# Kernel tuning notes

Measured on AMD Instinct MI355X. Metric: run time of the kernel, lower is better.

Reference implementation:

```python
import jax, jax.numpy as jnp
import numpy as np

B, S, D = 8, 1024, 1152
H = 16
HD = D // H
HID = int(D * 4.0)
LN_EPS = 1e-5


def layer_norm(x, w, b):
    m = jnp.mean(x, axis=-1, keepdims=True)
    v = jnp.mean(jnp.square(x - m), axis=-1, keepdims=True)
    return (x - m) * jax.lax.rsqrt(v + LN_EPS) * w + b


def modulate(x, shift, scale):
    # shift/scale: [B, D] broadcast over seq
    return x * (1.0 + scale[:, None, :]) + shift[:, None, :]


def setup_inputs() -> dict:
    key = jax.random.key(0)
    ks = jax.random.split(key, 16)
    s = 0.02
    return {
        "x": jax.random.normal(ks[0], (B, S, D), jnp.float32),
        "c": jax.random.normal(ks[1], (B, D), jnp.float32),
        "ln1_w": jnp.ones((D,), jnp.float32),
        "ln1_b": jnp.zeros((D,), jnp.float32),
        "wq": jax.random.normal(ks[2], (D, D), jnp.float32) * s,
        "wk": jax.random.normal(ks[3], (D, D), jnp.float32) * s,
        "wv": jax.random.normal(ks[4], (D, D), jnp.float32) * s,
        "wo": jax.random.normal(ks[5], (D, D), jnp.float32) * s,
        "wo_b": jnp.zeros((D,), jnp.float32),
        "ln2_w": jnp.ones((D,), jnp.float32),
        "ln2_b": jnp.zeros((D,), jnp.float32),
        "fc1_w": jax.random.normal(ks[6], (D, HID), jnp.float32) * s,
        "fc1_b": jnp.zeros((HID,), jnp.float32),
        "fc2_w": jax.random.normal(ks[7], (HID, D), jnp.float32) * s,
        "fc2_b": jnp.zeros((D,), jnp.float32),
        "ada_w": jax.random.normal(ks[8], (D, 6 * D), jnp.float32) * s,
        "ada_b": jnp.zeros((6 * D,), jnp.float32),
    }


def attention(x, wq, wk, wv, wo, wo_b):
    b, s, d = x.shape
    q = (x @ wq).reshape(b, s, H, HD).transpose(0, 2, 1, 3)  # [B,H,S,hd]
    k = (x @ wk).reshape(b, s, H, HD).transpose(0, 2, 1, 3)
    v = (x @ wv).reshape(b, s, H, HD).transpose(0, 2, 1, 3)
    scale = 1.0 / np.sqrt(HD).astype(np.float32)
    att = jnp.einsum("bhqd,bhkd->bhqk", q, k) * scale
    att = jax.nn.softmax(att, axis=-1)
    out = jnp.einsum("bhqk,bhkd->bhqd", att, v)
    out = out.transpose(0, 2, 1, 3).reshape(b, s, d)
    return out @ wo + wo_b


def reference(x, c, ln1_w, ln1_b, wq, wk, wv, wo, wo_b, ln2_w, ln2_b,
              fc1_w, fc1_b, fc2_w, fc2_b, ada_w, ada_b):
    mod = jax.nn.silu(c) @ ada_w + ada_b  # [B, 6D]
    sh_msa, sc_msa, g_msa, sh_mlp, sc_mlp, g_mlp = jnp.split(mod, 6, axis=1)
    h = modulate(layer_norm(x, ln1_w, ln1_b), sh_msa, sc_msa)
    x = x + g_msa[:, None, :] * attention(h, wq, wk, wv, wo, wo_b)
    h = modulate(layer_norm(x, ln2_w, ln2_b), sh_mlp, sc_mlp)
    h = jax.nn.gelu(h @ fc1_w + fc1_b, approximate=False) @ fc2_w + fc2_b
    x = x + g_mlp[:, None, :] * h
    return x
```

## Files before the change

kernel.cpp:

```cpp
#include <hip/hip_runtime.h>
#include <hip/hip_bf16.h>


typedef unsigned short u16;
typedef unsigned int u32;
typedef __attribute__((ext_vector_type(8))) short bf16x8;
typedef __attribute__((ext_vector_type(4))) float f32x4;

#define MFMA16(a, b, c) __builtin_amdgcn_mfma_f32_16x16x32_bf16((a), (b), (c), 0, 0, 0)

__device__ __forceinline__ u16 f2bf(float f) {
  __hip_bfloat16 h = __float2bfloat16(f);
  return __builtin_bit_cast(u16, h);
}

__device__ __forceinline__ void gload16(const u16* g, u16* l) {
  __builtin_amdgcn_global_load_lds(
      (const __attribute__((address_space(1))) unsigned int*)(const void*)g,
      (__attribute__((address_space(3))) unsigned int*)(void*)l, 16, 0, 0);
}

__global__ void k_silu(const float* __restrict__ c, float* __restrict__ o, int n) {
  int i = blockIdx.x * 256 + threadIdx.x;
  if (i < n) { float v = c[i]; o[i] = v / (1.f + __expf(-v)); }
}

__global__ __launch_bounds__(256) void k_modproj1(const float* __restrict__ sc,
                                                  const float* __restrict__ aw,
                                                  float* __restrict__ partial) {
  __shared__ float lc[8][144];
  int kc = blockIdx.y;
  for (int i = threadIdx.x; i < 1152; i += 256) {
    int b = i / 144, k = i % 144;
    lc[b][k] = sc[b * 1152 + kc * 144 + k];
  }
  __syncthreads();
  int j = blockIdx.x * 256 + threadIdx.x;
  float acc[8] = {0, 0, 0, 0, 0, 0, 0, 0};
  for (int k = 0; k < 144; ++k) {
    float w = aw[(size_t)(kc * 144 + k) * 6912 + j];
    #pragma unroll
    for (int b = 0; b < 8; ++b) acc[b] += lc[b][k] * w;
  }
  #pragma unroll
  for (int b = 0; b < 8; ++b) partial[((size_t)kc * 8 + b) * 6912 + j] = acc[b];
}

__global__ __launch_bounds__(256) void k_modproj2(const float* __restrict__ partial,
                                                  const float* __restrict__ ab,
                                                  float* __restrict__ mo) {
  int j = blockIdx.x * 256 + threadIdx.x;
  float bias = ab[j];
  #pragma unroll
  for (int b = 0; b < 8; ++b) {
    float s = 0.f;
    #pragma unroll
    for (int kc = 0; kc < 8; ++kc) s += partial[((size_t)kc * 8 + b) * 6912 + j];
    mo[(size_t)b * 6912 + j] = s + bias;
  }
}

__global__ __launch_bounds__(256) void k_tcvt(const float* __restrict__ in, u16* __restrict__ out,
                                              int K, int N) {
  __shared__ float t[32][33];
  int tx = threadIdx.x & 31, ty = threadIdx.x >> 5;
  size_t bx = (size_t)blockIdx.x * 32, by = (size_t)blockIdx.y * 32;
  #pragma unroll
  for (int i = 0; i < 4; ++i) t[ty + 8 * i][tx] = in[(by + ty + 8 * i) * N + bx + tx];
  __syncthreads();
  #pragma unroll
  for (int i = 0; i < 4; ++i) out[(bx + ty + 8 * i) * K + by + tx] = f2bf(t[tx][ty + 8 * i]);
}

__global__ __launch_bounds__(256) void k_lnmod(const float* __restrict__ xin,
                                               const float* __restrict__ w,
                                               const float* __restrict__ bs,
                                               const float* __restrict__ mo,
                                               int sh_off, int sc_off, u16* __restrict__ o) {
  int row = blockIdx.x;
  int b = row >> 10;
  int tid = threadIdx.x;
  const float4* x4 = (const float4*)(xin + (size_t)row * 1152);
  float4 v0 = x4[tid];
  float4 v1 = make_float4(0.f, 0.f, 0.f, 0.f);
  if (tid < 32) v1 = x4[256 + tid];
  float s = v0.x + v0.y + v0.z + v0.w + v1.x + v1.y + v1.z + v1.w;
  float sq = v0.x * v0.x + v0.y * v0.y + v0.z * v0.z + v0.w * v0.w +
             v1.x * v1.x + v1.y * v1.y + v1.z * v1.z + v1.w * v1.w;
  #pragma unroll
  for (int d = 32; d > 0; d >>= 1) { s += __shfl_down(s, d); sq += __shfl_down(sq, d); }
  __shared__ float ps[4], pq[4];
  int wid = tid >> 6, lane = tid & 63;
  if (lane == 0) { ps[wid] = s; pq[wid] = sq; }
  __syncthreads();
  float S = ps[0] + ps[1] + ps[2] + ps[3];
  float SQ = pq[0] + pq[1] + pq[2] + pq[3];
  float mean = S * (1.f / 1152.f);
  float var = SQ * (1.f / 1152.f) - mean * mean;
  float rs = rsqrtf(var + 1e-5f);
  const float* shp = mo + (size_t)b * 6912 + sh_off;
  const float* scp = mo + (size_t)b * 6912 + sc_off;
  u16* orow = o + (size_t)row * 1152;
  {
    int col = 4 * tid;
    ushort4 u; float y;
    y = (v0.x - mean) * rs * w[col + 0] + bs[col + 0]; u.x = f2bf(y * (1.f + scp[col + 0]) + shp[col + 0]);
    y = (v0.y - mean) * rs * w[col + 1] + bs[col + 1]; u.y = f2bf(y * (1.f + scp[col + 1]) + shp[col + 1]);
    y = (v0.z - mean) * rs * w[col + 2] + bs[col + 2]; u.z = f2bf(y * (1.f + scp[col + 2]) + shp[col + 2]);
    y = (v0.w - mean) * rs * w[col + 3] + bs[col + 3]; u.w = f2bf(y * (1.f + scp[col + 3]) + shp[col + 3]);
    *(ushort4*)&orow[col] = u;
  }
  if (tid < 32) {
    int col = 1024 + 4 * tid;
    ushort4 u; float y;
    y = (v1.x - mean) * rs * w[col + 0] + bs[col + 0]; u.x = f2bf(y * (1.f + scp[col + 0]) + shp[col + 0]);
    y = (v1.y - mean) * rs * w[col + 1] + bs[col + 1]; u.y = f2bf(y * (1.f + scp[col + 1]) + shp[col + 1]);
    y = (v1.z - mean) * rs * w[col + 2] + bs[col + 2]; u.z = f2bf(y * (1.f + scp[col + 2]) + shp[col + 2]);
    y = (v1.w - mean) * rs * w[col + 3] + bs[col + 3]; u.w = f2bf(y * (1.f + scp[col + 3]) + shp[col + 3]);
    *(ushort4*)&orow[col] = u;
  }
}

template <int EPI>
__global__ __launch_bounds__(256) void k_gemm(const u16* __restrict__ A, const u16* __restrict__ Bt,
                                              int Kst, int klen, u16* __restrict__ Cb,
                                              float* __restrict__ Cf,
                                              const float* __restrict__ bias,
                                              const float* __restrict__ res,
                                              const float* __restrict__ mo, int goff,
                                              u16* __restrict__ vt) {
  const int tid = threadIdx.x;
  const int w = tid >> 6, lane = tid & 63;
  const int wr = w >> 1, wc = w & 1;
  const int lr = lane & 15, kg = lane >> 4;

  const int nwg = gridDim.x * gridDim.y;
  const int id = blockIdx.y * gridDim.x + blockIdx.x;
  const int swz = (id & 7) * (nwg >> 3) + (id >> 3);
  const int tM = (swz / gridDim.x) * 128, tN = (swz % gridDim.x) * 128;
  const int N = gridDim.x * 128;
  const int koff = blockIdx.z * klen;

  __shared__ u16 lA[2][128 * 32];
  __shared__ u16 lB[2][128 * 32];
  f32x4 acc[4][4];
  #pragma unroll
  for (int m = 0; m < 4; ++m)
    #pragma unroll
    for (int n = 0; n < 4; ++n) acc[m][n] = f32x4{0.f, 0.f, 0.f, 0.f};

  const int lrow = lane >> 2, lseg = lane & 3;
  const u16* gA = A + (size_t)(tM + w * 32 + lrow) * Kst + lseg * 8 + koff;
  const u16* gB = Bt + (size_t)(tN + w * 32 + lrow) * Kst + lseg * 8 + koff;
  const size_t rstep = (size_t)16 * Kst;
  const int wo0 = (w * 32) * 32, wo1 = (w * 32 + 16) * 32;
  const int aoff = (wr * 64 + lr) * 32 + kg * 8;
  const int boff = (wc * 64 + lr) * 32 + kg * 8;

#define STAGE(buf, ks)                        \
  do {                                        \
    gload16(gA + (ks), lA[buf] + wo0);        \
    gload16(gA + rstep + (ks), lA[buf] + wo1);\
    gload16(gB + (ks), lB[buf] + wo0);        \
    gload16(gB + rstep + (ks), lB[buf] + wo1);\
  } while (0)

#define COMPUTE(buf)                                                                  \
  do {                                                                                \
    bf16x8 af[4], bfr[4];                                                             \
    _Pragma("unroll")                                                                 \
    for (int m = 0; m < 4; ++m) af[m] = *(const bf16x8*)&lA[buf][aoff + m * 16 * 32]; \
    _Pragma("unroll")                                                                 \
    for (int n = 0; n < 4; ++n) bfr[n] = *(const bf16x8*)&lB[buf][boff + n * 16 * 32];\
    _Pragma("unroll")                                                                 \
    for (int m = 0; m < 4; ++m)                                                       \
      _Pragma("unroll")                                                               \
      for (int n = 0; n < 4; ++n) acc[m][n] = MFMA16(af[m], bfr[n], acc[m][n]);       \
  } while (0)

  const int nt = klen >> 5;
  STAGE(0, 0);
  __syncthreads();
  int t = 1;
  for (; t + 1 < nt; t += 2) {
    STAGE(1, t * 32);
    COMPUTE(0);
    __syncthreads();
    STAGE(0, t * 32 + 32);
    COMPUTE(1);
    __syncthreads();
  }
  STAGE(1, t * 32);
  COMPUTE(0);
  __syncthreads();
  COMPUTE(1);
#undef STAGE
#undef COMPUTE

  if (EPI == 3) {
    #pragma unroll
    for (int m = 0; m < 4; ++m)
      #pragma unroll
      for (int n = 0; n < 4; ++n) {
        int gcol = tN + wc * 64 + n * 16 + lr;
        int s0 = tM + wr * 64 + m * 16 + kg * 4;
        if (tN < 2304) {
          #pragma unroll
          for (int r = 0; r < 4; ++r) Cb[(size_t)(s0 + r) * N + gcol] = f2bf(acc[m][n][r]);
        } else {
          int qq = gcol - 2304;
          int hh = qq / 72;
          int d = qq - hh * 72;
          int bb = s0 >> 10, sl = s0 & 1023;
          ushort4 u;
          u.x = f2bf(acc[m][n][0]); u.y = f2bf(acc[m][n][1]);
          u.z = f2bf(acc[m][n][2]); u.w = f2bf(acc[m][n][3]);
          *(ushort4*)&vt[(((size_t)bb * 16 + hh) * 72 + d) * 1024 + sl] = u;
        }
      }
  } else if (EPI == 4) {
    float* Po = Cf + (size_t)blockIdx.z * ((size_t)gridDim.y * 128) * N;
    #pragma unroll
    for (int m = 0; m < 4; ++m)
      #pragma unroll
      for (int n = 0; n < 4; ++n)
        #pragma unroll
        for (int r = 0; r < 4; ++r) {
          int grow = tM + wr * 64 + m * 16 + kg * 4 + r;
          int gcol = tN + wc * 64 + n * 16 + lr;
          Po[(size_t)grow * N + gcol] = acc[m][n][r];
        }
  } else {
    #pragma unroll
    for (int m = 0; m < 4; ++m)
      #pragma unroll
      for (int n = 0; n < 4; ++n)
        #pragma unroll
        for (int r = 0; r < 4; ++r) {
          int grow = tM + wr * 64 + m * 16 + kg * 4 + r;
          int gcol = tN + wc * 64 + n * 16 + lr;
          size_t idx = (size_t)grow * N + gcol;
          float v = acc[m][n][r];
          if (EPI == 1) {
            float g = mo[(size_t)(grow >> 10) * 6912 + goff + gcol];
            Cf[idx] = res[idx] + g * (v + bias[gcol]);
          } else {
            float z = v + bias[gcol];
            float z2 = z * z;
            float u = z * __fmaf_rn(z2, -0.0713548162f, -1.5957691216f);
            float e = __expf(u);
            float gel = z * __builtin_amdgcn_rcpf(1.f + e);
            Cb[idx] = f2bf(gel);
          }
        }
  }
}

__global__ __launch_bounds__(256) void k_fc2red(const float* __restrict__ p,
                                                const float* __restrict__ x1,
                                                const float* __restrict__ bias,
                                                const float* __restrict__ mo,
                                                float* __restrict__ out) {
  size_t i = ((size_t)blockIdx.x * 256 + threadIdx.x) * 4;
  int row = (int)(i / 1152);
  int col = (int)(i - (size_t)row * 1152);
  int b = row >> 10;
  float4 a0 = *(const float4*)(p + i);
  float4 a1 = *(const float4*)(p + 9437184ull + i);
  float4 r = *(const float4*)(x1 + i);
  const float* gp = mo + (size_t)b * 6912 + 5760 + col;
  const float* bp = bias + col;
  float4 o;
  o.x = r.x + gp[0] * (a0.x + a1.x + bp[0]);
  o.y = r.y + gp[1] * (a0.y + a1.y + bp[1]);
  o.z = r.z + gp[2] * (a0.z + a1.z + bp[2]);
  o.w = r.w + gp[3] * (a0.w + a1.w + bp[3]);
  *(float4*)(out + i) = o;
}

__global__ __launch_bounds__(256) void k_attn(const u16* __restrict__ QKV, const u16* __restrict__ Vt,
                                              u16* __restrict__ O) {
  const int tid = threadIdx.x;
  const int w = tid >> 6, lane = tid & 63;
  const int lr = lane & 15, kg = lane >> 4;
  int bx = blockIdx.x;
  bx = (bx & 7) * 256 + (bx >> 3);
  const int qt = bx & 15, h = (bx >> 4) & 15, b = bx >> 8;

  __shared__ u16 lQ[64][104];
  __shared__ u16 lK[64][104];
  __shared__ u16 lVt[80][72];
  __shared__ u16 lPt[4][16][72];

  const size_t qkbase = (size_t)b * 1024 * 3456 + (size_t)h * 72;
  const u16* Qg = QKV + qkbase;
  const u16* Kg = QKV + qkbase + 1152;
  const u16* Vg = Vt + ((size_t)(b * 16 + h) * 72) * 1024;

  const uint4 z4 = make_uint4(0, 0, 0, 0);
  for (int L = tid; L < 192; L += 256) {
    int r = L / 3, s = L - (L / 3) * 3;
    *(uint4*)&lQ[r][72 + s * 8] = z4;
    *(uint4*)&lK[r][72 + s * 8] = z4;
  }
  for (int L = tid; L < 72; L += 256) {
    int r = L / 9, s = L - (L / 9) * 9;
    *(uint4*)&lVt[72 + r][s * 8] = z4;
  }
  {
    int L = tid; int r = L / 9, s = L - r * 9;
    *(uint4*)&lQ[r][s * 8] = *(const uint4*)(Qg + (size_t)(qt * 64 + r) * 3456 + s * 8);
    L = tid + 256; r = L / 9; s = L - r * 9;
    *(uint4*)&lQ[r][s * 8] = *(const uint4*)(Qg + (size_t)(qt * 64 + r) * 3456 + s * 8);
    if (tid < 64) {
      L = tid + 512; r = L / 9; s = L - r * 9;
      *(uint4*)&lQ[r][s * 8] = *(const uint4*)(Qg + (size_t)(qt * 64 + r) * 3456 + s * 8);
    }
  }
  __syncthreads();

  bf16x8 bq[3];
  #pragma unroll
  for (int ks = 0; ks < 3; ++ks) bq[ks] = *(const bf16x8*)&lQ[w * 16 + lr][ks * 32 + kg * 8];

  const float scale = 0.11785113019775793f;
  float mrun = -1e30f, lrun = 0.f;
  f32x4 oacc[5];
  #pragma unroll
  for (int nd = 0; nd < 5; ++nd) oacc[nd] = f32x4{0.f, 0.f, 0.f, 0.f};

  for (int kt = 0; kt < 16; ++kt) {
    __syncthreads();
    {
      int L = tid; int r = L / 9, s = L - (L / 9) * 9;
      *(uint4*)&lK[r][s * 8] = *(const uint4*)(Kg + (size_t)(kt * 64 + r) * 3456 + s * 8);
      int d = tid >> 3, sg = tid & 7;
      *(uint4*)&lVt[d][sg * 8] = *(const uint4*)(Vg + (size_t)d * 1024 + kt * 64 + sg * 8);
      L = tid + 256; r = L / 9; s = L - r * 9;
      *(uint4*)&lK[r][s * 8] = *(const uint4*)(Kg + (size_t)(kt * 64 + r) * 3456 + s * 8);
      d = (tid + 256) >> 3; sg = tid & 7;
      *(uint4*)&lVt[d][sg * 8] = *(const uint4*)(Vg + (size_t)d * 1024 + kt * 64 + sg * 8);
      if (tid < 64) {
        L = tid + 512; r = L / 9; s = L - r * 9;
        *(uint4*)&lK[r][s * 8] = *(const uint4*)(Kg + (size_t)(kt * 64 + r) * 3456 + s * 8);
        d = (tid + 512) >> 3;
        *(uint4*)&lVt[d][sg * 8] = *(const uint4*)(Vg + (size_t)d * 1024 + kt * 64 + sg * 8);
      }
    }
    __syncthreads();

    f32x4 sfr[4];
    __builtin_amdgcn_s_setprio(1);
    #pragma unroll
    for (int kb = 0; kb < 4; ++kb) {
      f32x4 sv = f32x4{0.f, 0.f, 0.f, 0.f};
      #pragma unroll
      for (int ks = 0; ks < 3; ++ks) {
        bf16x8 ak = *(const bf16x8*)&lK[kb * 16 + lr][ks * 32 + kg * 8];
        sv = MFMA16(ak, bq[ks], sv);
      }
      sfr[kb] = sv;
    }
    __builtin_amdgcn_s_setprio(0);

    float mx = sfr[0][0];
    #pragma unroll
    for (int kb = 0; kb < 4; ++kb)
      #pragma unroll
      for (int r = 0; r < 4; ++r) mx = fmaxf(mx, sfr[kb][r]);
    mx = fmaxf(mx, __shfl_xor(mx, 16));
    mx = fmaxf(mx, __shfl_xor(mx, 32));
    mx *= scale;
    float mn = fmaxf(mrun, mx);
    float al = __expf(mrun - mn);
    mrun = mn;
    float sum = 0.f;
    #pragma unroll
    for (int kb = 0; kb < 4; ++kb) {
      #pragma unroll
      for (int rp = 0; rp < 2; ++rp) {
        float p0 = __expf(__fmaf_rn(sfr[kb][2 * rp], scale, -mn));
        float p1 = __expf(__fmaf_rn(sfr[kb][2 * rp + 1], scale, -mn));
        sum += p0 + p1;
        u32 pk = (u32)f2bf(p0) | ((u32)f2bf(p1) << 16);
        *(u32*)&lPt[w][lr][kb * 16 + kg * 4 + rp * 2] = pk;
      }
    }
    sum += __shfl_xor(sum, 16);
    sum += __shfl_xor(sum, 32);
    lrun = lrun * al + sum;
    #pragma unroll
    for (int nd = 0; nd < 5; ++nd)
      #pragma unroll
      for (int r = 0; r < 4; ++r) oacc[nd][r] *= al;

    __builtin_amdgcn_s_setprio(1);
    #pragma unroll
    for (int s = 0; s < 2; ++s) {
      bf16x8 bp = *(const bf16x8*)&lPt[w][lr][s * 32 + kg * 8];
      #pragma unroll
      for (int nd = 0; nd < 5; ++nd) {
        bf16x8 av = *(const bf16x8*)&lVt[nd * 16 + lr][s * 32 + kg * 8];
        oacc[nd] = MFMA16(av, bp, oacc[nd]);
      }
    }
    __builtin_amdgcn_s_setprio(0);
  }

  float inv = 1.f / lrun;
  size_t orow = ((size_t)b * 1024 + qt * 64 + w * 16 + lr) * 1152 + h * 72;
  #pragma unroll
  for (int nd = 0; nd < 5; ++nd) {
    int d0 = nd * 16 + kg * 4;
    if (d0 < 72) {
      ushort4 u;
      u.x = f2bf(oacc[nd][0] * inv);
      u.y = f2bf(oacc[nd][1] * inv);
      u.z = f2bf(oacc[nd][2] * inv);
      u.w = f2bf(oacc[nd][3] * inv);
      *(ushort4*)&O[orow + d0] = u;
    }
  }
}

extern "C" void kernel_launch(void* const* d_in, const int* in_sizes, int n_in,
                              void* d_out, int out_size, void* d_ws, size_t ws_size,
                              hipStream_t stream) {
  const float* x     = (const float*)d_in[0];
  const float* c     = (const float*)d_in[1];
  const float* ln1_w = (const float*)d_in[2];
  const float* ln1_b = (const float*)d_in[3];
  const float* wq    = (const float*)d_in[4];
  const float* wk    = (const float*)d_in[5];
  const float* wv    = (const float*)d_in[6];
  const float* wo    = (const float*)d_in[7];
  const float* wo_b  = (const float*)d_in[8];
  const float* ln2_w = (const float*)d_in[9];
  const float* ln2_b = (const float*)d_in[10];
  const float* fc1_w = (const float*)d_in[11];
  const float* fc1_b = (const float*)d_in[12];
  const float* fc2_w = (const float*)d_in[13];
  const float* fc2_b = (const float*)d_in[14];
  const float* ada_w = (const float*)d_in[15];
  const float* ada_b = (const float*)d_in[16];
  float* out = (float*)d_out;

  char* base = (char*)d_ws;
  size_t off = 0;
  auto alloc = [&](size_t nbytes) -> void* {
    void* p = base + off;
    off += (nbytes + 255) & ~(size_t)255;
    return p;
  };
  const size_t MD = 8192ull * 1152;
  float* silu_c = (float*)alloc(9216 * 4);
  float* partial = (float*)alloc(64ull * 6912 * 4);
  float* modb   = (float*)alloc(55296 * 4);
  u16* qkvT = (u16*)alloc(3456ull * 1152 * 2);
  u16* woT  = (u16*)alloc(1152ull * 1152 * 2);
  u16* fc1T = (u16*)alloc(4608ull * 1152 * 2);
  u16* fc2T = (u16*)alloc(1152ull * 4608 * 2);
  u16* hbuf = (u16*)alloc(MD * 2);
  float* x1 = (float*)alloc(MD * 4);
  u16* vtb  = (u16*)alloc(128ull * 72 * 1024 * 2);
  float* fc2p = (float*)alloc(2ull * MD * 4);
  u16* big  = (u16*)alloc(8192ull * 4608 * 2);
  u16* qkv = big;
  u16* m1 = big;

  k_silu<<<36, 256, 0, stream>>>(c, silu_c, 9216);
  k_modproj1<<<dim3(27, 8), 256, 0, stream>>>(silu_c, ada_w, partial);
  k_modproj2<<<27, 256, 0, stream>>>(partial, ada_b, modb);
  k_tcvt<<<dim3(36, 36), 256, 0, stream>>>(wq, qkvT, 1152, 1152);
  k_tcvt<<<dim3(36, 36), 256, 0, stream>>>(wk, qkvT + 1152ull * 1152, 1152, 1152);
  k_tcvt<<<dim3(36, 36), 256, 0, stream>>>(wv, qkvT + 2304ull * 1152, 1152, 1152);
  k_tcvt<<<dim3(36, 36), 256, 0, stream>>>(wo, woT, 1152, 1152);
  k_tcvt<<<dim3(144, 36), 256, 0, stream>>>(fc1_w, fc1T, 1152, 4608);
  k_tcvt<<<dim3(36, 144), 256, 0, stream>>>(fc2_w, fc2T, 4608, 1152);

  k_lnmod<<<8192, 256, 0, stream>>>(x, ln1_w, ln1_b, modb, 0, 1152, hbuf);
  k_gemm<3><<<dim3(27, 64), 256, 0, stream>>>(hbuf, qkvT, 1152, 1152, qkv, nullptr, nullptr, nullptr, nullptr, 0, vtb);
  k_attn<<<2048, 256, 0, stream>>>(qkv, vtb, hbuf);
  k_gemm<1><<<dim3(9, 64), 256, 0, stream>>>(hbuf, woT, 1152, 1152, nullptr, x1, wo_b, x, modb, 2304, nullptr);
  k_lnmod<<<8192, 256, 0, stream>>>(x1, ln2_w, ln2_b, modb, 3456, 4608, hbuf);
  k_gemm<2><<<dim3(36, 64), 256, 0, stream>>>(hbuf, fc1T, 1152, 1152, m1, nullptr, fc1_b, nullptr, nullptr, 0, nullptr);
  k_gemm<4><<<dim3(9, 64, 2), 256, 0, stream>>>(m1, fc2T, 4608, 2304, nullptr, fc2p, nullptr, nullptr, nullptr, 0, nullptr);
  k_fc2red<<<9216, 256, 0, stream>>>(fc2p, x1, fc2_b, modb, out);
}
```

Baseline: 603.2 us.

## Triple-buffer GEMM LDS pipeline with vmcnt waits and XOR-swizzled layout

Moves the bf16 GEMM main loop from double to triple buffering in LDS. It replaces __syncthreads with explicit s_waitcnt vmcnt(4) plus a barrier, so two tiles of global loads stay in flight while the current tile is computed. It also XOR-swizzles the 16-byte k-segments in LDS, applied on both the global-load source and the fragment reads, to reduce bank conflicts. The loop now assumes the k-tile count is a multiple of three, and the extra buffer raises LDS use, which may lower occupancy.

```diff
diff --git a/kernel.cpp b/kernel.cpp
--- a/kernel.cpp
+++ b/kernel.cpp
@@ -141,8 +141,8 @@
   const int N = gridDim.x * 128;
   const int koff = blockIdx.z * klen;
 
-  __shared__ u16 lA[2][128 * 32];
-  __shared__ u16 lB[2][128 * 32];
+  __shared__ u16 lA[3][128 * 32];
+  __shared__ u16 lB[3][128 * 32];
   f32x4 acc[4][4];
   #pragma unroll
   for (int m = 0; m < 4; ++m)
@@ -150,12 +150,14 @@
     for (int n = 0; n < 4; ++n) acc[m][n] = f32x4{0.f, 0.f, 0.f, 0.f};
 
   const int lrow = lane >> 2, lseg = lane & 3;
-  const u16* gA = A + (size_t)(tM + w * 32 + lrow) * Kst + lseg * 8 + koff;
-  const u16* gB = Bt + (size_t)(tN + w * 32 + lrow) * Kst + lseg * 8 + koff;
+  const int fl = (lrow & 3) ^ ((lrow >> 2) & 3);
+  const u16* gA = A + (size_t)(tM + w * 32 + lrow) * Kst + (lseg ^ fl) * 8 + koff;
+  const u16* gB = Bt + (size_t)(tN + w * 32 + lrow) * Kst + (lseg ^ fl) * 8 + koff;
   const size_t rstep = (size_t)16 * Kst;
   const int wo0 = (w * 32) * 32, wo1 = (w * 32 + 16) * 32;
-  const int aoff = (wr * 64 + lr) * 32 + kg * 8;
-  const int boff = (wc * 64 + lr) * 32 + kg * 8;
+  const int flane = (lr & 3) ^ ((lr >> 2) & 3);
+  const int aoff = (wr * 64 + lr) * 32 + (kg ^ flane) * 8;
+  const int boff = (wc * 64 + lr) * 32 + (kg ^ flane) * 8;
 
 #define STAGE(buf, ks)                        \
   do {                                        \
@@ -178,24 +180,29 @@
       for (int n = 0; n < 4; ++n) acc[m][n] = MFMA16(af[m], bfr[n], acc[m][n]);       \
   } while (0)
 
+#define WAITBAR(Nst)                                          \
+  do {                                                        \
+    asm volatile("s_waitcnt vmcnt(" #Nst ")" ::: "memory");   \
+    __builtin_amdgcn_s_barrier();                             \
+    __builtin_amdgcn_sched_barrier(0);                        \
+  } while (0)
+
   const int nt = klen >> 5;
   STAGE(0, 0);
-  __syncthreads();
-  int t = 1;
-  for (; t + 1 < nt; t += 2) {
-    STAGE(1, t * 32);
-    COMPUTE(0);
-    __syncthreads();
-    STAGE(0, t * 32 + 32);
-    COMPUTE(1);
-    __syncthreads();
-  }
-  STAGE(1, t * 32);
-  COMPUTE(0);
-  __syncthreads();
-  COMPUTE(1);
+  STAGE(1, 32);
+  int ks = 64;
+  for (int g = 0; g < nt / 3 - 1; ++g) {
+    WAITBAR(4); STAGE(2, ks);      COMPUTE(0);
+    WAITBAR(4); STAGE(0, ks + 32); COMPUTE(1);
+    WAITBAR(4); STAGE(1, ks + 64); COMPUTE(2);
+    ks += 96;
+  }
+  WAITBAR(4); STAGE(2, ks); COMPUTE(0);
+  WAITBAR(4); COMPUTE(1);
+  WAITBAR(0); COMPUTE(2);
 #undef STAGE
 #undef COMPUTE
+#undef WAITBAR
 
   if (EPI == 3) {
     #pragma unroll
```

Result: no change. 615.0 us (+2.0%).
